# Kernel optimization log

Hardware: AMD Instinct MI355X
Metric: run time of the kernel (lower is better)

The kernel has to match this reference:

```python
import jax, jax.numpy as jnp
import numpy as np

GAMMA = 0.99
LAM = 0.95
CLIP = 0.2
VALUE_COEFF = 0.5
ENTROPY_COEFF = 0.01
T = 500_000
S = 128
A = 16


def _mlp(x, W1, b1, W2, b2, W3, b3):
    h = jax.nn.relu(x @ W1 + b1)
    h = jax.nn.relu(h @ W2 + b2)
    return h @ W3 + b3


def setup_inputs() -> dict:
    key = jax.random.key(0)
    ks = jax.random.split(key, 12)
    states = jax.random.normal(ks[0], (T, S), dtype=jnp.float32)
    next_states = jax.random.normal(ks[1], (T, S), dtype=jnp.float32)
    rewards = jax.random.normal(ks[2], (T,), dtype=jnp.float32)
    dones = (jax.random.uniform(ks[3], (T,)) < 0.01).astype(jnp.float32)
    actions = jax.random.randint(ks[4], (T,), 0, A)
    # old log-probs of taken actions (valid log-probabilities)
    old_logp = jnp.log(jax.random.uniform(ks[5], (T,), minval=1e-3, maxval=1.0))

    def lin(k, fan_in, fan_out):
        lim = 1.0 / np.sqrt(fan_in)
        return jax.random.uniform(k, (fan_in, fan_out), minval=-lim, maxval=lim, dtype=jnp.float32)

    return {
        'states': states, 'next_states': next_states, 'rewards': rewards,
        'dones': dones, 'actions': actions, 'old_logp': old_logp,
        'aW1': lin(ks[6], S, 64), 'ab1': jnp.zeros((64,), jnp.float32),
        'aW2': lin(ks[7], 64, 64), 'ab2': jnp.zeros((64,), jnp.float32),
        'aW3': lin(ks[8], 64, A), 'ab3': jnp.zeros((A,), jnp.float32),
        'cW1': lin(ks[9], S, 64), 'cb1': jnp.zeros((64,), jnp.float32),
        'cW2': lin(ks[10], 64, 64), 'cb2': jnp.zeros((64,), jnp.float32),
        'cW3': lin(ks[11], 64, 1), 'cb3': jnp.zeros((1,), jnp.float32),
    }


def reference(states, next_states, rewards, dones, actions, old_logp,
              aW1, ab1, aW2, ab2, aW3, ab3,
              cW1, cb1, cW2, cb2, cW3, cb3):
    # ---- critic values and TD deltas ----
    values = _mlp(states, cW1, cb1, cW2, cb2, cW3, cb3)[:, 0]        # [T]
    next_values = _mlp(next_states, cW1, cb1, cW2, cb2, cW3, cb3)[:, 0]
    not_done = 1.0 - dones
    deltas = rewards + GAMMA * next_values * not_done - values       # [T]

    # ---- GAE: reverse-time linear recurrence a_t = c_t * a_{t+1} + d_t ----
    coef = GAMMA * LAM * not_done

    def step(carry, cd):
        c, d = cd
        a = c * carry + d
        return a, a

    _, advantages = jax.lax.scan(step, jnp.float32(0.0), (coef, deltas), reverse=True)
    returns = advantages + values
    adv_n = (advantages - advantages.mean()) / (jnp.std(advantages, ddof=1) + 1e-8)

    # ---- actor: clipped surrogate ----
    probs = jax.nn.softmax(_mlp(states, aW1, ab1, aW2, ab2, aW3, ab3), axis=-1)  # [T, A]
    logp = jnp.log(jnp.take_along_axis(probs, actions[:, None], axis=1))[:, 0]   # [T]
    ratios = jnp.exp(logp - old_logp)
    surr1 = ratios * adv_n
    surr2 = jnp.clip(ratios, 1.0 - CLIP, 1.0 + CLIP) * adv_n
    actor_loss = -jnp.minimum(surr1, surr2).mean()

    # ---- critic MSE loss ----
    critic_loss = jnp.mean((values - returns) ** 2)

    # ---- entropy bonus ----
    entropy_loss = jnp.mean(-jnp.sum(probs * jnp.log(probs + 1e-8), axis=-1))

    total_loss = actor_loss + VALUE_COEFF * critic_loss - ENTROPY_COEFF * entropy_loss
    return jnp.stack([total_loss, actor_loss, critic_loss, entropy_loss])
```

## Files before the change

kernel.cpp:

```cpp
#include <hip/hip_runtime.h>
#include <hip/hip_bf16.h>

#define T_N 500000
#define NTILE 31250
#define NBLK 768
#define NWAVES (NBLK * 4)
#define NCHUNK 4096
#define CHUNKL 128
#define NPART 1024

typedef __attribute__((ext_vector_type(8))) short short8v;
typedef __attribute__((ext_vector_type(4))) float float4v;

__device__ __forceinline__ short f2bf(float f) {
    __hip_bfloat16 b = __float2bfloat16(f);
    return *reinterpret_cast<short*>(&b);
}

__device__ __forceinline__ short8v cvt8(const float4 a, const float4 b) {
    short8v r;
    r[0] = f2bf(a.x); r[1] = f2bf(a.y); r[2] = f2bf(a.z); r[3] = f2bf(a.w);
    r[4] = f2bf(b.x); r[5] = f2bf(b.y); r[6] = f2bf(b.z); r[7] = f2bf(b.w);
    return r;
}

#define FC1 0
#define FA1 16
#define FC2 32
#define FA2 40
#define FA3 48
#define NFRAG 50

__global__ __launch_bounds__(64) void k_pack(
    const float* __restrict__ cW1, const float* __restrict__ aW1,
    const float* __restrict__ cW2, const float* __restrict__ aW2,
    const float* __restrict__ aW3, short8v* __restrict__ packed)
{
    const int f = blockIdx.x, l = threadIdx.x;
    const int g = l >> 4, col = l & 15;
    const float* W; int s, c, ncol;
    if (f < FA1)      { W = cW1; s = f >> 2;         c = f & 3;         ncol = 64; }
    else if (f < FC2) { W = aW1; s = (f - FA1) >> 2; c = (f - FA1) & 3; ncol = 64; }
    else if (f < FA2) { W = cW2; s = (f - FC2) >> 2; c = (f - FC2) & 3; ncol = 64; }
    else if (f < FA3) { W = aW2; s = (f - FA2) >> 2; c = (f - FA2) & 3; ncol = 64; }
    else              { W = aW3; s = f - FA3;        c = 0;             ncol = 16; }
    short8v frag;
    #pragma unroll
    for (int j = 0; j < 8; ++j) {
        int k = s * 32 + g * 8 + j;
        frag[j] = f2bf(W[k * ncol + c * 16 + col]);
    }
    packed[f * 64 + l] = frag;
}

__device__ __forceinline__ void store_h(short (*hb)[68], const float4v* acc, int g, int q) {
    #pragma unroll
    for (int c = 0; c < 4; ++c)
        #pragma unroll
        for (int r = 0; r < 4; ++r)
            hb[g * 4 + r][c * 16 + q] = f2bf(fmaxf(acc[c][r], 0.f));
}

__global__ __launch_bounds__(256) void k_mlp(
    const float* __restrict__ states, const float* __restrict__ next_states,
    const float* __restrict__ rewards, const float* __restrict__ dones,
    const int* __restrict__ actions, const float* __restrict__ old_logp,
    const short8v* __restrict__ pk,
    const float* __restrict__ cb1, const float* __restrict__ ab1,
    const float* __restrict__ cb2, const float* __restrict__ ab2,
    const float* __restrict__ ab3,
    const float* __restrict__ cW3, const float* __restrict__ cb3,
    float* __restrict__ delta_o, float* __restrict__ coef_o,
    float* __restrict__ ratio_o, float* __restrict__ ent_o)
{
    __shared__ __align__(16) short hlds[4][2][16][68];
    const int wv = threadIdx.x >> 6, l = threadIdx.x & 63;
    const int g = l >> 4, q = l & 15;
    short (*h0)[68] = hlds[wv][0];
    short (*h1)[68] = hlds[wv][1];

    int tile = blockIdx.x * 4 + wv;
    if (tile >= NTILE) return;

    float4 rs[8], rn[8];
    {
        const float* xs = states + ((long long)tile * 16 + q) * 128 + g * 8;
        const float* xn = next_states + ((long long)tile * 16 + q) * 128 + g * 8;
        #pragma unroll
        for (int s = 0; s < 4; ++s) {
            rs[2 * s]     = *reinterpret_cast<const float4*>(xs + s * 32);
            rs[2 * s + 1] = *reinterpret_cast<const float4*>(xs + s * 32 + 4);
            rn[2 * s]     = *reinterpret_cast<const float4*>(xn + s * 32);
            rn[2 * s + 1] = *reinterpret_cast<const float4*>(xn + s * 32 + 4);
        }
    }

    while (true) {
        const int next = tile + NWAVES;
        const long long r0 = (long long)tile * 16;

        short8v sa[4], na[4];
        #pragma unroll
        for (int s = 0; s < 4; ++s) {
            sa[s] = cvt8(rs[2 * s], rs[2 * s + 1]);
            na[s] = cvt8(rn[2 * s], rn[2 * s + 1]);
        }

        if (next < NTILE) {
            const float* xs = states + ((long long)next * 16 + q) * 128 + g * 8;
            const float* xn = next_states + ((long long)next * 16 + q) * 128 + g * 8;
            #pragma unroll
            for (int s = 0; s < 4; ++s) {
                rs[2 * s]     = *reinterpret_cast<const float4*>(xs + s * 32);
                rs[2 * s + 1] = *reinterpret_cast<const float4*>(xs + s * 32 + 4);
                rn[2 * s]     = *reinterpret_cast<const float4*>(xn + s * 32);
                rn[2 * s + 1] = *reinterpret_cast<const float4*>(xn + s * 32 + 4);
            }
        }

        float4v accC[4], accN[4];
        #pragma unroll
        for (int c = 0; c < 4; ++c) {
            float b = cb1[c * 16 + q];
            accC[c] = (float4v){b, b, b, b};
            accN[c] = accC[c];
        }
        #pragma unroll
        for (int s = 0; s < 4; ++s) {
            #pragma unroll
            for (int c = 0; c < 4; ++c) {
                short8v w = pk[(FC1 + s * 4 + c) * 64 + l];
                accC[c] = __builtin_amdgcn_mfma_f32_16x16x32_bf16(sa[s], w, accC[c], 0, 0, 0);
                accN[c] = __builtin_amdgcn_mfma_f32_16x16x32_bf16(na[s], w, accN[c], 0, 0, 0);
            }
        }
        store_h(h0, accC, g, q);
        store_h(h1, accN, g, q);

        float4v c2C[4], c2N[4];
        #pragma unroll
        for (int c = 0; c < 4; ++c) {
            float b = cb2[c * 16 + q];
            c2C[c] = (float4v){b, b, b, b};
            c2N[c] = c2C[c];
        }
        #pragma unroll
        for (int s = 0; s < 2; ++s) {
            short8v aC = *reinterpret_cast<const short8v*>(&h0[q][s * 32 + g * 8]);
            short8v aN = *reinterpret_cast<const short8v*>(&h1[q][s * 32 + g * 8]);
            #pragma unroll
            for (int c = 0; c < 4; ++c) {
                short8v w = pk[(FC2 + s * 4 + c) * 64 + l];
                c2C[c] = __builtin_amdgcn_mfma_f32_16x16x32_bf16(aC, w, c2C[c], 0, 0, 0);
                c2N[c] = __builtin_amdgcn_mfma_f32_16x16x32_bf16(aN, w, c2N[c], 0, 0, 0);
            }
        }
        float vr[4] = {0.f, 0.f, 0.f, 0.f}, nr[4] = {0.f, 0.f, 0.f, 0.f};
        #pragma unroll
        for (int c = 0; c < 4; ++c) {
            float w3 = cW3[c * 16 + q];
            #pragma unroll
            for (int r = 0; r < 4; ++r) {
                vr[r] = fmaf(fmaxf(c2C[c][r], 0.f), w3, vr[r]);
                nr[r] = fmaf(fmaxf(c2N[c][r], 0.f), w3, nr[r]);
            }
        }
        #pragma unroll
        for (int o = 1; o < 16; o <<= 1)
            #pragma unroll
            for (int r = 0; r < 4; ++r) {
                vr[r] += __shfl_xor(vr[r], o);
                nr[r] += __shfl_xor(nr[r], o);
            }
        const float cb3v = cb3[0];
        float v[4], nv[4];
        #pragma unroll
        for (int r = 0; r < 4; ++r) { v[r] = vr[r] + cb3v; nv[r] = nr[r] + cb3v; }

        float4v aA[4];
        #pragma unroll
        for (int c = 0; c < 4; ++c) { float b = ab1[c * 16 + q]; aA[c] = (float4v){b, b, b, b}; }
        #pragma unroll
        for (int s = 0; s < 4; ++s)
            #pragma unroll
            for (int c = 0; c < 4; ++c)
                aA[c] = __builtin_amdgcn_mfma_f32_16x16x32_bf16(sa[s], pk[(FA1 + s * 4 + c) * 64 + l], aA[c], 0, 0, 0);
        store_h(h0, aA, g, q);

        float4v a2[4];
        #pragma unroll
        for (int c = 0; c < 4; ++c) { float b = ab2[c * 16 + q]; a2[c] = (float4v){b, b, b, b}; }
        #pragma unroll
        for (int s = 0; s < 2; ++s) {
            short8v aa = *reinterpret_cast<const short8v*>(&h0[q][s * 32 + g * 8]);
            #pragma unroll
            for (int c = 0; c < 4; ++c)
                a2[c] = __builtin_amdgcn_mfma_f32_16x16x32_bf16(aa, pk[(FA2 + s * 4 + c) * 64 + l], a2[c], 0, 0, 0);
        }
        store_h(h1, a2, g, q);

        const float b3 = ab3[q];
        float4v a3 = (float4v){b3, b3, b3, b3};
        #pragma unroll
        for (int s = 0; s < 2; ++s) {
            short8v aa = *reinterpret_cast<const short8v*>(&h1[q][s * 32 + g * 8]);
            a3 = __builtin_amdgcn_mfma_f32_16x16x32_bf16(aa, pk[(FA3 + s) * 64 + l], a3, 0, 0, 0);
        }

        float lg[4], mx[4], pe[4], se[4], tt[4], ent[4], logp[4];
        #pragma unroll
        for (int r = 0; r < 4; ++r) { lg[r] = a3[r]; mx[r] = lg[r]; }
        #pragma unroll
        for (int o = 1; o < 16; o <<= 1)
            #pragma unroll
            for (int r = 0; r < 4; ++r) mx[r] = fmaxf(mx[r], __shfl_xor(mx[r], o));
        #pragma unroll
        for (int r = 0; r < 4; ++r) {
            pe[r] = __expf(lg[r] - mx[r]);
            se[r] = pe[r];
            tt[r] = pe[r] * lg[r];
        }
        #pragma unroll
        for (int o = 1; o < 16; o <<= 1)
            #pragma unroll
            for (int r = 0; r < 4; ++r) {
                se[r] += __shfl_xor(se[r], o);
                tt[r] += __shfl_xor(tt[r], o);
            }
        const int4 av = *reinterpret_cast<const int4*>(&actions[r0 + g * 4]);
        const int act[4] = {av.x, av.y, av.z, av.w};
        #pragma unroll
        for (int r = 0; r < 4; ++r) {
            float ls = __logf(se[r]);
            ent[r] = mx[r] + ls - tt[r] / se[r];
            float sel = __shfl(lg[r], (l & 48) | act[r]);
            logp[r] = sel - mx[r] - ls;
        }

        if (q == 0) {
            const long long rb = r0 + g * 4;
            const float4 rw = *reinterpret_cast<const float4*>(&rewards[rb]);
            const float4 dn = *reinterpret_cast<const float4*>(&dones[rb]);
            const float4 ol = *reinterpret_cast<const float4*>(&old_logp[rb]);
            const float rwv[4] = {rw.x, rw.y, rw.z, rw.w};
            const float dnv[4] = {dn.x, dn.y, dn.z, dn.w};
            const float olv[4] = {ol.x, ol.y, ol.z, ol.w};
            const float GL = 0.99f * 0.95f;
            float dl[4], cf[4], rt[4];
            #pragma unroll
            for (int r = 0; r < 4; ++r) {
                float nd = 1.f - dnv[r];
                dl[r] = fmaf(0.99f * nd, nv[r], rwv[r]) - v[r];
                cf[r] = GL * nd;
                rt[r] = __expf(logp[r] - olv[r]);
            }
            float4 t;
            t.x = dl[0]; t.y = dl[1]; t.z = dl[2]; t.w = dl[3];
            *reinterpret_cast<float4*>(&delta_o[rb]) = t;
            t.x = cf[0]; t.y = cf[1]; t.z = cf[2]; t.w = cf[3];
            *reinterpret_cast<float4*>(&coef_o[rb]) = t;
            t.x = rt[0]; t.y = rt[1]; t.z = rt[2]; t.w = rt[3];
            *reinterpret_cast<float4*>(&ratio_o[rb]) = t;
            t.x = ent[0]; t.y = ent[1]; t.z = ent[2]; t.w = ent[3];
            *reinterpret_cast<float4*>(&ent_o[rb]) = t;
        }

        if (next >= NTILE) break;
        tile = next;
    }
}

__global__ __launch_bounds__(256) void k_gae_chunk(
    const float* __restrict__ coef, const float* __restrict__ delta,
    float* __restrict__ P, float* __restrict__ Q)
{
    const int c = blockIdx.x * 256 + threadIdx.x;
    const long long lo = (long long)c * CHUNKL;
    float p = 1.f, a = 0.f;
    if (lo < T_N) {
        const int n = (int)((T_N - lo < CHUNKL) ? (T_N - lo) : CHUNKL);
        for (int j = (n >> 2) - 1; j >= 0; --j) {
            float4 cfv = *reinterpret_cast<const float4*>(&coef[lo + 4 * j]);
            float4 dlv = *reinterpret_cast<const float4*>(&delta[lo + 4 * j]);
            a = fmaf(cfv.w, a, dlv.w);
            a = fmaf(cfv.z, a, dlv.z);
            a = fmaf(cfv.y, a, dlv.y);
            a = fmaf(cfv.x, a, dlv.x);
            p *= cfv.x * cfv.y * cfv.z * cfv.w;
        }
    }
    P[c] = p; Q[c] = a;
}

__global__ __launch_bounds__(1024) void k_gae_scan(
    const float* __restrict__ P, const float* __restrict__ Q,
    float* __restrict__ carry)
{
    __shared__ float sp[1024], sq[1024];
    const int t = threadIdx.x, b = t * 4;
    float p = P[b + 3], q = Q[b + 3];
    #pragma unroll
    for (int c = 2; c >= 0; --c) {
        float pc = P[b + c], qc = Q[b + c];
        q = fmaf(pc, q, qc);
        p = pc * p;
    }
    sp[t] = p; sq[t] = q;
    __syncthreads();
    for (int d = 1; d < 1024; d <<= 1) {
        float pp = sp[t], qq = sq[t];
        float p2 = 1.f, q2 = 0.f;
        const bool has = (t + d) < 1024;
        if (has) { p2 = sp[t + d]; q2 = sq[t + d]; }
        __syncthreads();
        if (has) { sp[t] = pp * p2; sq[t] = fmaf(pp, q2, qq); }
        __syncthreads();
    }
    float x = (t + 1 < 1024) ? sq[t + 1] : 0.f;
    #pragma unroll
    for (int c = 3; c >= 0; --c) {
        carry[b + c] = x;
        x = fmaf(P[b + c], x, Q[b + c]);
    }
}

__global__ __launch_bounds__(256) void k_gae_apply(
    const float* __restrict__ coef, const float* __restrict__ delta,
    const float* __restrict__ carry, float* __restrict__ adv,
    float* __restrict__ part)
{
    const int c = blockIdx.x * 256 + threadIdx.x;
    const long long lo = (long long)c * CHUNKL;
    float s = 0.f, s2 = 0.f;
    if (lo < T_N) {
        const int n = (int)((T_N - lo < CHUNKL) ? (T_N - lo) : CHUNKL);
        float a = carry[c];
        for (int j = (n >> 2) - 1; j >= 0; --j) {
            float4 cfv = *reinterpret_cast<const float4*>(&coef[lo + 4 * j]);
            float4 dlv = *reinterpret_cast<const float4*>(&delta[lo + 4 * j]);
            float a3 = fmaf(cfv.w, a, dlv.w);
            float a2v = fmaf(cfv.z, a3, dlv.z);
            float a1 = fmaf(cfv.y, a2v, dlv.y);
            float a0 = fmaf(cfv.x, a1, dlv.x);
            float4 o; o.x = a0; o.y = a1; o.z = a2v; o.w = a3;
            *reinterpret_cast<float4*>(&adv[lo + 4 * j]) = o;
            a = a0;
            s += a0 + a1 + a2v + a3;
            s2 += a0 * a0 + a1 * a1 + a2v * a2v + a3 * a3;
        }
    }
    #pragma unroll
    for (int o = 32; o > 0; o >>= 1) { s += __shfl_down(s, o); s2 += __shfl_down(s2, o); }
    __shared__ float l0[4], l1[4];
    const int wv = threadIdx.x >> 6, ln = threadIdx.x & 63;
    if (ln == 0) { l0[wv] = s; l1[wv] = s2; }
    __syncthreads();
    if (threadIdx.x == 0) {
        part[blockIdx.x * 2]     = l0[0] + l0[1] + l0[2] + l0[3];
        part[blockIdx.x * 2 + 1] = l1[0] + l1[1] + l1[2] + l1[3];
    }
}

__global__ __launch_bounds__(256) void k_actor(
    const float* __restrict__ adv, const float* __restrict__ ratio,
    const float* __restrict__ ent, const float* __restrict__ part,
    float* __restrict__ part4)
{
    __shared__ float st[2];
    if (threadIdx.x == 0) {
        float S = 0.f, S2 = 0.f;
        #pragma unroll
        for (int i = 0; i < 16; ++i) { S += part[2 * i]; S2 += part[2 * i + 1]; }
        const float Tf = (float)T_N;
        float mean = S / Tf;
        float var = (S2 - S * S / Tf) / (Tf - 1.f);
        st[0] = mean;
        st[1] = 1.f / (sqrtf(fmaxf(var, 0.f)) + 1e-8f);
    }
    __syncthreads();
    const float mean = st[0], isd = st[1];
    float sm = 0.f, se = 0.f;
    for (long long i = (long long)blockIdx.x * 256 + threadIdx.x; i < T_N;
         i += (long long)gridDim.x * 256) {
        float an = (adv[i] - mean) * isd;
        float rt = ratio[i];
        float s1 = rt * an;
        float s2v = fminf(fmaxf(rt, 0.8f), 1.2f) * an;
        sm += fminf(s1, s2v);
        se += ent[i];
    }
    #pragma unroll
    for (int o = 32; o > 0; o >>= 1) { sm += __shfl_down(sm, o); se += __shfl_down(se, o); }
    __shared__ float l0[4], l1[4];
    const int wv = threadIdx.x >> 6, ln = threadIdx.x & 63;
    if (ln == 0) { l0[wv] = sm; l1[wv] = se; }
    __syncthreads();
    if (threadIdx.x == 0) {
        part4[blockIdx.x * 2]     = l0[0] + l0[1] + l0[2] + l0[3];
        part4[blockIdx.x * 2 + 1] = l1[0] + l1[1] + l1[2] + l1[3];
    }
}

__global__ __launch_bounds__(1024) void k_final(
    const float* __restrict__ part4, const float* __restrict__ part,
    float* __restrict__ out)
{
    const int t = threadIdx.x;
    float sm = part4[t * 2], se = part4[t * 2 + 1];
    #pragma unroll
    for (int o = 32; o > 0; o >>= 1) { sm += __shfl_down(sm, o); se += __shfl_down(se, o); }
    __shared__ float l0[16], l1[16];
    const int wv = t >> 6, ln = t & 63;
    if (ln == 0) { l0[wv] = sm; l1[wv] = se; }
    __syncthreads();
    if (t == 0) {
        float SM = 0.f, SE = 0.f;
        #pragma unroll
        for (int i = 0; i < 16; ++i) { SM += l0[i]; SE += l1[i]; }
        float S2 = 0.f;
        #pragma unroll
        for (int i = 0; i < 16; ++i) S2 += part[2 * i + 1];
        const float Tf = (float)T_N;
        float actor_loss = -SM / Tf;
        float ent_loss = SE / Tf;
        float critic_loss = S2 / Tf;
        float total = actor_loss + 0.5f * critic_loss - 0.01f * ent_loss;
        out[0] = total; out[1] = actor_loss; out[2] = critic_loss; out[3] = ent_loss;
    }
}

extern "C" void kernel_launch(void* const* d_in, const int* in_sizes, int n_in,
                              void* d_out, int out_size, void* d_ws, size_t ws_size,
                              hipStream_t stream) {
    (void)in_sizes; (void)n_in; (void)out_size; (void)ws_size;
    const float* states      = (const float*)d_in[0];
    const float* next_states = (const float*)d_in[1];
    const float* rewards     = (const float*)d_in[2];
    const float* dones       = (const float*)d_in[3];
    const int*   actions     = (const int*)d_in[4];
    const float* old_logp    = (const float*)d_in[5];
    const float* aW1 = (const float*)d_in[6];  const float* ab1 = (const float*)d_in[7];
    const float* aW2 = (const float*)d_in[8];  const float* ab2 = (const float*)d_in[9];
    const float* aW3 = (const float*)d_in[10]; const float* ab3 = (const float*)d_in[11];
    const float* cW1 = (const float*)d_in[12]; const float* cb1 = (const float*)d_in[13];
    const float* cW2 = (const float*)d_in[14]; const float* cb2 = (const float*)d_in[15];
    const float* cW3 = (const float*)d_in[16]; const float* cb3 = (const float*)d_in[17];
    float* out = (float*)d_out;

    float* ws = (float*)d_ws;
    float* delta = ws;
    float* coef  = ws + 1 * (size_t)T_N;
    float* ratio = ws + 2 * (size_t)T_N;
    float* entb  = ws + 3 * (size_t)T_N;
    float* adv   = ws + 4 * (size_t)T_N;
    float* P     = ws + 5 * (size_t)T_N;
    float* Q     = P + NCHUNK;
    float* carry = Q + NCHUNK;
    float* part  = carry + NCHUNK;
    float* part4 = part + 32;
    short8v* packed = (short8v*)(part4 + 2048);

    k_pack<<<NFRAG, 64, 0, stream>>>(cW1, aW1, cW2, aW2, aW3, packed);
    k_mlp<<<NBLK, 256, 0, stream>>>(
        states, next_states, rewards, dones, actions, old_logp, packed,
        cb1, ab1, cb2, ab2, ab3, cW3, cb3, delta, coef, ratio, entb);
    k_gae_chunk<<<NCHUNK / 256, 256, 0, stream>>>(coef, delta, P, Q);
    k_gae_scan<<<1, 1024, 0, stream>>>(P, Q, carry);
    k_gae_apply<<<NCHUNK / 256, 256, 0, stream>>>(coef, delta, carry, adv, part);
    k_actor<<<NPART, 256, 0, stream>>>(adv, ratio, entb, part, part4);
    k_final<<<1, 1024, 0, stream>>>(part4, part, out);
}
```

Before: 225.7 us.

## Stage packed MLP weights in LDS and hoist bias loads out of tile loop

Each block copies the packed bf16 weight fragments into shared memory once, and the MFMA loops then read B operands from LDS instead of global/L2. The per-tile bias and cW3 loads move into registers before the persistent loop. The grid shrinks from 768 to 512 blocks so fewer blocks each pay the weight staging cost. The larger LDS footprint may reduce occupancy, and the smaller grid gives each wave more tiles to process.

```diff
diff --git a/kernel.cpp b/kernel.cpp
--- a/kernel.cpp
+++ b/kernel.cpp
@@ -3,7 +3,7 @@
 
 #define T_N 500000
 #define NTILE 31250
-#define NBLK 768
+#define NBLK 512
 #define NWAVES (NBLK * 4)
 #define NCHUNK 4096
 #define CHUNKL 128
@@ -73,14 +73,30 @@
     float* __restrict__ delta_o, float* __restrict__ coef_o,
     float* __restrict__ ratio_o, float* __restrict__ ent_o)
 {
+    __shared__ __align__(16) short8v spk[NFRAG * 64];
     __shared__ __align__(16) short hlds[4][2][16][68];
     const int wv = threadIdx.x >> 6, l = threadIdx.x & 63;
     const int g = l >> 4, q = l & 15;
     short (*h0)[68] = hlds[wv][0];
     short (*h1)[68] = hlds[wv][1];
 
+    for (int i = threadIdx.x; i < NFRAG * 64; i += 256) spk[i] = pk[i];
+    __syncthreads();
+
     int tile = blockIdx.x * 4 + wv;
     if (tile >= NTILE) return;
+
+    float bc1[4], bc2[4], ba1[4], ba2[4], w3[4];
+    #pragma unroll
+    for (int c = 0; c < 4; ++c) {
+        bc1[c] = cb1[c * 16 + q];
+        bc2[c] = cb2[c * 16 + q];
+        ba1[c] = ab1[c * 16 + q];
+        ba2[c] = ab2[c * 16 + q];
+        w3[c]  = cW3[c * 16 + q];
+    }
+    const float ab3q = ab3[q];
+    const float cb3v = cb3[0];
 
     float4 rs[8], rn[8];
     {
@@ -121,15 +137,14 @@
         float4v accC[4], accN[4];
         #pragma unroll
         for (int c = 0; c < 4; ++c) {
-            float b = cb1[c * 16 + q];
-            accC[c] = (float4v){b, b, b, b};
+            accC[c] = (float4v){bc1[c], bc1[c], bc1[c], bc1[c]};
             accN[c] = accC[c];
         }
         #pragma unroll
         for (int s = 0; s < 4; ++s) {
             #pragma unroll
             for (int c = 0; c < 4; ++c) {
-                short8v w = pk[(FC1 + s * 4 + c) * 64 + l];
+                short8v w = spk[(FC1 + s * 4 + c) * 64 + l];
                 accC[c] = __builtin_amdgcn_mfma_f32_16x16x32_bf16(sa[s], w, accC[c], 0, 0, 0);
                 accN[c] = __builtin_amdgcn_mfma_f32_16x16x32_bf16(na[s], w, accN[c], 0, 0, 0);
             }
@@ -140,8 +155,7 @@
         float4v c2C[4], c2N[4];
         #pragma unroll
         for (int c = 0; c < 4; ++c) {
-            float b = cb2[c * 16 + q];
-            c2C[c] = (float4v){b, b, b, b};
+            c2C[c] = (float4v){bc2[c], bc2[c], bc2[c], bc2[c]};
             c2N[c] = c2C[c];
         }
         #pragma unroll
@@ -150,7 +164,7 @@
             short8v aN = *reinterpret_cast<const short8v*>(&h1[q][s * 32 + g * 8]);
             #pragma unroll
             for (int c = 0; c < 4; ++c) {
-                short8v w = pk[(FC2 + s * 4 + c) * 64 + l];
+                short8v w = spk[(FC2 + s * 4 + c) * 64 + l];
                 c2C[c] = __builtin_amdgcn_mfma_f32_16x16x32_bf16(aC, w, c2C[c], 0, 0, 0);
                 c2N[c] = __builtin_amdgcn_mfma_f32_16x16x32_bf16(aN, w, c2N[c], 0, 0, 0);
             }
@@ -158,11 +172,10 @@
         float vr[4] = {0.f, 0.f, 0.f, 0.f}, nr[4] = {0.f, 0.f, 0.f, 0.f};
         #pragma unroll
         for (int c = 0; c < 4; ++c) {
-            float w3 = cW3[c * 16 + q];
             #pragma unroll
             for (int r = 0; r < 4; ++r) {
-                vr[r] = fmaf(fmaxf(c2C[c][r], 0.f), w3, vr[r]);
-                nr[r] = fmaf(fmaxf(c2N[c][r], 0.f), w3, nr[r]);
+                vr[r] = fmaf(fmaxf(c2C[c][r], 0.f), w3[c], vr[r]);
+                nr[r] = fmaf(fmaxf(c2N[c][r], 0.f), w3[c], nr[r]);
             }
         }
         #pragma unroll
@@ -172,39 +185,37 @@
                 vr[r] += __shfl_xor(vr[r], o);
                 nr[r] += __shfl_xor(nr[r], o);
             }
-        const float cb3v = cb3[0];
         float v[4], nv[4];
         #pragma unroll
         for (int r = 0; r < 4; ++r) { v[r] = vr[r] + cb3v; nv[r] = nr[r] + cb3v; }
 
         float4v aA[4];
         #pragma unroll
-        for (int c = 0; c < 4; ++c) { float b = ab1[c * 16 + q]; aA[c] = (float4v){b, b, b, b}; }
+        for (int c = 0; c < 4; ++c) aA[c] = (float4v){ba1[c], ba1[c], ba1[c], ba1[c]};
         #pragma unroll
         for (int s = 0; s < 4; ++s)
             #pragma unroll
             for (int c = 0; c < 4; ++c)
-                aA[c] = __builtin_amdgcn_mfma_f32_16x16x32_bf16(sa[s], pk[(FA1 + s * 4 + c) * 64 + l], aA[c], 0, 0, 0);
+                aA[c] = __builtin_amdgcn_mfma_f32_16x16x32_bf16(sa[s], spk[(FA1 + s * 4 + c) * 64 + l], aA[c], 0, 0, 0);
         store_h(h0, aA, g, q);
 
         float4v a2[4];
         #pragma unroll
-        for (int c = 0; c < 4; ++c) { float b = ab2[c * 16 + q]; a2[c] = (float4v){b, b, b, b}; }
+        for (int c = 0; c < 4; ++c) a2[c] = (float4v){ba2[c], ba2[c], ba2[c], ba2[c]};
         #pragma unroll
         for (int s = 0; s < 2; ++s) {
             short8v aa = *reinterpret_cast<const short8v*>(&h0[q][s * 32 + g * 8]);
             #pragma unroll
             for (int c = 0; c < 4; ++c)
-                a2[c] = __builtin_amdgcn_mfma_f32_16x16x32_bf16(aa, pk[(FA2 + s * 4 + c) * 64 + l], a2[c], 0, 0, 0);
+                a2[c] = __builtin_amdgcn_mfma_f32_16x16x32_bf16(aa, spk[(FA2 + s * 4 + c) * 64 + l], a2[c], 0, 0, 0);
         }
         store_h(h1, a2, g, q);
 
-        const float b3 = ab3[q];
-        float4v a3 = (float4v){b3, b3, b3, b3};
+        float4v a3 = (float4v){ab3q, ab3q, ab3q, ab3q};
         #pragma unroll
         for (int s = 0; s < 2; ++s) {
             short8v aa = *reinterpret_cast<const short8v*>(&h1[q][s * 32 + g * 8]);
-            a3 = __builtin_amdgcn_mfma_f32_16x16x32_bf16(aa, pk[(FA3 + s) * 64 + l], a3, 0, 0, 0);
+            a3 = __builtin_amdgcn_mfma_f32_16x16x32_bf16(aa, spk[(FA3 + s) * 64 + l], a3, 0, 0, 0);
         }
 
         float lg[4], mx[4], pe[4], se[4], tt[4], ent[4], logp[4];
```

Result: faster. 211.8 us (-6.2%).
